# Kernel tuning notes

Measured on AMD Instinct MI355X. Metric: run time of the kernel, lower is better.

## Reference

```python
import jax, jax.numpy as jnp
import numpy as np

T, B, S = 720, 50000, 7  # timesteps, num_series, seasonality


def setup_inputs() -> dict:
    key = jax.random.key(0)
    k1, k2, k3, k4 = jax.random.split(key, 4)
    # positive data so divisions/logs are well-behaved (HW smoothing assumes positive series)
    train_padded = jax.random.uniform(k1, (T, B), jnp.float32, 0.5, 1.5)
    init_lev_sms = jax.random.uniform(k2, (B,), jnp.float32)
    init_seas_sms = jax.random.uniform(k3, (B,), jnp.float32)
    init_seasonalities = jax.random.uniform(k4, (B, S), jnp.float32)
    return {
        "train_padded": train_padded,
        "init_lev_sms": init_lev_sms,
        "init_seas_sms": init_seas_sms,
        "init_seasonalities": init_seasonalities,
    }


def _esrnn_smoothing(train_padded, init_lev_sms, init_seas_sms, init_seasonalities):
    # sigmoid of per-series smoothing params (idxs == arange(num_series))
    lev_sm = jax.nn.sigmoid(init_lev_sms)    # [B]
    seas_sm = jax.nn.sigmoid(init_seas_sms)  # [B]
    S_ = init_seasonalities.shape[1]
    init_seas = jnp.exp(init_seasonalities)  # [B, S]
    seas0_dup = init_seas[:, 0]              # seasonalities list gets exp(init[:,0]) appended again

    lev0 = train_padded[0] / init_seas[:, 0]  # [B]
    # ring buffer holding seasonalities[i .. i+S-1]; at loop start (i=1) holds indices 1..S
    buf0 = jnp.concatenate([init_seas[:, 1:].T, seas0_dup[None, :]], axis=0)  # [S, B]

    xs = (train_padded[1:], jnp.arange(1, train_padded.shape[0]))

    def step(carry, x_i):
        lev_prev, buf = carry
        x, i = x_i
        pos = (i - 1) % S_
        s_i = buf[pos]  # seasonalities[i]
        new_lev = lev_sm * (x / s_i) + (1.0 - lev_sm) * lev_prev
        log_diff = jnp.log(new_lev / lev_prev)
        new_seas = seas_sm * (x / new_lev) + (1.0 - seas_sm) * s_i  # seasonalities[i+S]
        buf = buf.at[pos].set(new_seas)
        return (new_lev, buf), (new_lev, log_diff, new_seas)

    (_, _), (levs_tail, log_diffs, seas_tail) = jax.lax.scan(step, (lev0, buf0), xs)

    levs = jnp.concatenate([lev0[None, :], levs_tail], axis=0)  # [T, B]
    seas_head = jnp.concatenate([init_seas.T, seas0_dup[None, :]], axis=0)  # [S+1, B]
    seasonalities_stacked = jnp.concatenate([seas_head, seas_tail], axis=0)  # [T+S, B]
    # level variability penalty term: mean over series of squared 2nd log-diff
    sq_log_diff = (log_diffs[1:] - log_diffs[:-1]) ** 2  # [T-2, B]
    mean_sq_log_diff = jnp.mean(sq_log_diff, axis=1)     # [T-2]
    return levs, seasonalities_stacked, mean_sq_log_diff


def reference(train_padded, init_lev_sms, init_seas_sms, init_seasonalities):
    return _esrnn_smoothing(train_padded, init_lev_sms, init_seas_sms, init_seasonalities)
```

## Files before the change

### kernel.cpp

```cpp
#include <hip/hip_runtime.h>

#define T_DIM 720
#define B_DIM 50000

#define OFF_SEAS (T_DIM * B_DIM)
#define SEAS_ROWS 727
#define OFF_MSLD (OFF_SEAS + SEAS_ROWS * B_DIM)
#define N_MSLD 718

#define NBLK 782
#define NW NBLK
#define LN2_SQ 0.4804530139182014f

__device__ __forceinline__ float dpp_sum64(float v) {
#define DPP_ADD_STAGE(CTRL, RMASK)                                             \
  v += __int_as_float(__builtin_amdgcn_update_dpp(0, __float_as_int(v),        \
                                                  CTRL, RMASK, 0xf, false));
  DPP_ADD_STAGE(0x111, 0xf)
  DPP_ADD_STAGE(0x112, 0xf)
  DPP_ADD_STAGE(0x114, 0xf)
  DPP_ADD_STAGE(0x118, 0xf)
  DPP_ADD_STAGE(0x142, 0xa)
  DPP_ADD_STAGE(0x143, 0xc)
#undef DPP_ADD_STAGE
  return v;
}

#define PREFETCH(QB, G)                                                        \
  {                                                                            \
    int tp = 1 + 7 * (G);                                                      \
    _Pragma("unroll") for (int j = 0; j < 7; ++j) {                            \
      int r = tp + j;                                                          \
      r = r > 719 ? 719 : r;                                                   \
      QB[j] = __builtin_nontemporal_load(&train[r * B_DIM + bc]);              \
    }                                                                          \
  }

#define ESRNN_GROUP_N(QB, NS)                                                  \
  {                                                                            \
    float xds[7], nlv[7], llv[7];                                              \
    _Pragma("unroll") for (int j = 0; j < (NS); ++j)                           \
        xds[j] = __fdividef(QB[j], buf[j]);                                    \
    nlv[0] = fmaf(lsm, xds[0], olm * lev);                                     \
    _Pragma("unroll") for (int j = 1; j < (NS); ++j)                           \
        nlv[j] = fmaf(lsm, xds[j], olm * nlv[j - 1]);                          \
    _Pragma("unroll") for (int j = 0; j < (NS); ++j)                           \
        llv[j] = __log2f(nlv[j]);                                              \
    _Pragma("unroll") for (int j = 0; j < (NS); ++j) {                         \
      float ns = fmaf(ssm, __fdividef(QB[j], nlv[j]), osm * buf[j]);           \
      buf[j] = ns;                                                             \
    }                                                                          \
    if (valid) {                                                               \
      _Pragma("unroll") for (int j = 0; j < (NS); ++j) {                       \
        *(float*)(lbase + boff + (unsigned)(j * B_DIM * 4)) = nlv[j];          \
        *(float*)(sbase + boff + (unsigned)(j * B_DIM * 4)) = buf[j];          \
      }                                                                        \
    }                                                                          \
    boff += (NS)*B_DIM * 4;                                                    \
    float sqv[7];                                                              \
    {                                                                          \
      float ld0 = llv[0] - llev;                                               \
      float d0 = ld0 - pld;                                                    \
      sqv[0] = valid ? d0 * d0 : 0.0f;                                         \
      float ldp = ld0;                                                         \
      _Pragma("unroll") for (int j = 1; j < (NS); ++j) {                       \
        float ld = llv[j] - llv[j - 1];                                        \
        float d = ld - ldp;                                                    \
        sqv[j] = valid ? d * d : 0.0f;                                         \
        ldp = ld;                                                              \
      }                                                                        \
      pld = ldp;                                                               \
    }                                                                          \
    llev = llv[(NS)-1];                                                        \
    lev = nlv[(NS)-1];                                                         \
    _Pragma("unroll") for (int j = 0; j < (NS); ++j)                           \
        sqv[j] = dpp_sum64(sqv[j]);                                            \
    if (lane == 63) {                                                          \
      int tb = 1 + 7 * g;                                                      \
      _Pragma("unroll") for (int j = 0; j < (NS); ++j) {                       \
        int row = tb + j - 2;                                                  \
        if (row >= 0) partial[row * NW + wid] = sqv[j];                        \
      }                                                                        \
    }                                                                          \
  }

#define ESRNN_GROUP(QB, QP)                                                    \
  {                                                                            \
    PREFETCH(QP, g + 2)                                                        \
    ESRNN_GROUP_N(QB, 7)                                                       \
    ++g;                                                                       \
  }

__global__ __launch_bounds__(64) void esrnn_main(
    const float* __restrict__ train,
    const float* __restrict__ lev_sms,
    const float* __restrict__ seas_sms,
    const float* __restrict__ init_seas_in,
    float* __restrict__ levs_out,
    float* __restrict__ seas_out,
    float* __restrict__ partial)
{
  int b = blockIdx.x * 64 + threadIdx.x;
  bool valid = (b < B_DIM);
  int bc = valid ? b : (B_DIM - 1);
  int lane = threadIdx.x;
  int wid = blockIdx.x;

  float lsm = 1.0f / (1.0f + __expf(-lev_sms[bc]));
  float ssm = 1.0f / (1.0f + __expf(-seas_sms[bc]));
  float olm = 1.0f - lsm;
  float osm = 1.0f - ssm;

  float is[7];
#pragma unroll
  for (int j = 0; j < 7; ++j) is[j] = __expf(init_seas_in[bc * 7 + j]);

  float seas0 = is[0];
  float x0 = train[bc];
  float lev = __fdividef(x0, seas0);

  if (valid) {
    levs_out[b] = lev;
#pragma unroll
    for (int j = 0; j < 7; ++j) seas_out[j * B_DIM + b] = is[j];
    seas_out[7 * B_DIM + b] = seas0;
  }

  float buf[7];
#pragma unroll
  for (int j = 0; j < 6; ++j) buf[j] = is[j + 1];
  buf[6] = seas0;

  float llev = __log2f(lev);
  float pld = 0.0f;

  char* lbase = (char*)levs_out + (size_t)B_DIM * 4;
  char* sbase = (char*)seas_out + (size_t)8 * B_DIM * 4;
  unsigned int boff = (unsigned int)b * 4u;

  float xa[7], xb[7], xc[7];
  int g = 0;
  PREFETCH(xa, 0)
  PREFETCH(xb, 1)

  for (int k = 0; k < 34; ++k) {
    ESRNN_GROUP(xa, xc)
    ESRNN_GROUP(xb, xa)
    ESRNN_GROUP(xc, xb)
  }

  ESRNN_GROUP_N(xa, 5)
}

__global__ __launch_bounds__(64) void esrnn_reduce2(
    const float* __restrict__ partial, float* __restrict__ msld) {
  int row = blockIdx.x;
  int lane = threadIdx.x;
  float s = 0.0f;
  for (int i = lane; i < NW; i += 64) s += partial[row * NW + i];
  float tot = dpp_sum64(s);
  if (lane == 63) msld[row] = tot * (LN2_SQ / (float)B_DIM);
}

extern "C" void kernel_launch(void* const* d_in, const int* in_sizes, int n_in,
                              void* d_out, int out_size, void* d_ws,
                              size_t ws_size, hipStream_t stream) {
  const float* train = (const float*)d_in[0];
  const float* lev_sms = (const float*)d_in[1];
  const float* seas_sms = (const float*)d_in[2];
  const float* init_seas = (const float*)d_in[3];

  float* out = (float*)d_out;
  float* levs = out;
  float* seas = out + OFF_SEAS;
  float* msld = out + OFF_MSLD;
  float* partial = (float*)d_ws;

  esrnn_main<<<NBLK, 64, 0, stream>>>(train, lev_sms, seas_sms, init_seas,
                                      levs, seas, partial);
  esrnn_reduce2<<<N_MSLD, 64, 0, stream>>>(partial, msld);
}
```

Before: 125.5 us.

## Deepen load prefetch to three groups and defer wave reductions by one group

Loads of the training series now run three groups ahead using four rotating register buffers instead of two ahead with three. The cross-lane DPP reductions of the squared log-diffs are delayed by one group, using ping-pong accumulators, so they overlap with the next group's dependent recurrence chain. Nontemporal loads are replaced with plain loads. The change raises register pressure and shifts the partial-row indexing, and the epilogue has to handle the leftover groups explicitly.

```diff
diff --git a/kernel.cpp b/kernel.cpp
--- a/kernel.cpp
+++ b/kernel.cpp
@@ -32,11 +32,11 @@
     _Pragma("unroll") for (int j = 0; j < 7; ++j) {                            \
       int r = tp + j;                                                          \
       r = r > 719 ? 719 : r;                                                   \
-      QB[j] = __builtin_nontemporal_load(&train[r * B_DIM + bc]);              \
+      QB[j] = train[r * B_DIM + bc];                                           \
     }                                                                          \
   }
 
-#define ESRNN_GROUP_N(QB, NS)                                                  \
+#define ESRNN_COMPUTE(QB, SQC, NS)                                             \
   {                                                                            \
     float xds[7], nlv[7], llv[7];                                              \
     _Pragma("unroll") for (int j = 0; j < (NS); ++j)                           \
@@ -46,10 +46,8 @@
         nlv[j] = fmaf(lsm, xds[j], olm * nlv[j - 1]);                          \
     _Pragma("unroll") for (int j = 0; j < (NS); ++j)                           \
         llv[j] = __log2f(nlv[j]);                                              \
-    _Pragma("unroll") for (int j = 0; j < (NS); ++j) {                         \
-      float ns = fmaf(ssm, __fdividef(QB[j], nlv[j]), osm * buf[j]);           \
-      buf[j] = ns;                                                             \
-    }                                                                          \
+    _Pragma("unroll") for (int j = 0; j < (NS); ++j)                           \
+        buf[j] = fmaf(ssm, __fdividef(QB[j], nlv[j]), osm * buf[j]);           \
     if (valid) {                                                               \
       _Pragma("unroll") for (int j = 0; j < (NS); ++j) {                       \
         *(float*)(lbase + boff + (unsigned)(j * B_DIM * 4)) = nlv[j];          \
@@ -57,37 +55,39 @@
       }                                                                        \
     }                                                                          \
     boff += (NS)*B_DIM * 4;                                                    \
-    float sqv[7];                                                              \
     {                                                                          \
       float ld0 = llv[0] - llev;                                               \
       float d0 = ld0 - pld;                                                    \
-      sqv[0] = valid ? d0 * d0 : 0.0f;                                         \
+      SQC[0] = valid ? d0 * d0 : 0.0f;                                         \
       float ldp = ld0;                                                         \
       _Pragma("unroll") for (int j = 1; j < (NS); ++j) {                       \
         float ld = llv[j] - llv[j - 1];                                        \
         float d = ld - ldp;                                                    \
-        sqv[j] = valid ? d * d : 0.0f;                                         \
+        SQC[j] = valid ? d * d : 0.0f;                                         \
         ldp = ld;                                                              \
       }                                                                        \
       pld = ldp;                                                               \
     }                                                                          \
     llev = llv[(NS)-1];                                                        \
     lev = nlv[(NS)-1];                                                         \
-    _Pragma("unroll") for (int j = 0; j < (NS); ++j)                           \
-        sqv[j] = dpp_sum64(sqv[j]);                                            \
+  }
+
+#define ESRNN_REDUCE(SQ, NS, TB)                                               \
+  {                                                                            \
+    _Pragma("unroll") for (int j = 0; j < (NS); ++j) SQ[j] = dpp_sum64(SQ[j]); \
     if (lane == 63) {                                                          \
-      int tb = 1 + 7 * g;                                                      \
       _Pragma("unroll") for (int j = 0; j < (NS); ++j) {                       \
-        int row = tb + j - 2;                                                  \
-        if (row >= 0) partial[row * NW + wid] = sqv[j];                        \
+        int row = (TB) + j;                                                    \
+        if (row >= 0) partial[row * NW + wid] = SQ[j];                         \
       }                                                                        \
     }                                                                          \
   }
 
-#define ESRNN_GROUP(QB, QP)                                                    \
+#define ESRNN_GROUP(QB, QP, SQC, SQP)                                          \
   {                                                                            \
-    PREFETCH(QP, g + 2)                                                        \
-    ESRNN_GROUP_N(QB, 7)                                                       \
+    PREFETCH(QP, g + 3)                                                        \
+    ESRNN_COMPUTE(QB, SQC, 7)                                                  \
+    ESRNN_REDUCE(SQP, 7, 7 * g - 8)                                            \
     ++g;                                                                       \
   }
 
@@ -138,18 +138,27 @@
   char* sbase = (char*)seas_out + (size_t)8 * B_DIM * 4;
   unsigned int boff = (unsigned int)b * 4u;
 
-  float xa[7], xb[7], xc[7];
+  float xa[7], xb[7], xc[7], xd[7], sqa[7], sqb[7];
+#pragma unroll
+  for (int j = 0; j < 7; ++j) sqb[j] = 0.0f;
+
   int g = 0;
   PREFETCH(xa, 0)
   PREFETCH(xb, 1)
+  PREFETCH(xc, 2)
 
-  for (int k = 0; k < 34; ++k) {
-    ESRNN_GROUP(xa, xc)
-    ESRNN_GROUP(xb, xa)
-    ESRNN_GROUP(xc, xb)
+  for (int k = 0; k < 25; ++k) {
+    ESRNN_GROUP(xa, xd, sqa, sqb)
+    ESRNN_GROUP(xb, xa, sqb, sqa)
+    ESRNN_GROUP(xc, xb, sqa, sqb)
+    ESRNN_GROUP(xd, xc, sqb, sqa)
   }
+  ESRNN_GROUP(xa, xd, sqa, sqb)
+  ESRNN_GROUP(xb, xa, sqb, sqa)
 
-  ESRNN_GROUP_N(xa, 5)
+  ESRNN_REDUCE(sqb, 7, 706)
+  ESRNN_COMPUTE(xc, sqa, 5)
+  ESRNN_REDUCE(sqa, 5, 713)
 }
 
 __global__ __launch_bounds__(64) void esrnn_reduce2(
```

New measurement: 134.2 us. +6.9%, slower.
